# Kernel optimization log

Measured on AMD Instinct MI355X. Metric: run time of the kernel, lower is better.

Reference implementation:

```python
import jax, jax.numpy as jnp
import numpy as np

B, CDD, L, T, H, NH = 16, 10, 64, 128, 768, 12
DH = H // NH          # head dim = 64
S = CDD * L + T       # full sequence = 768 (640 candidate tokens + 128 terms)


def setup_inputs() -> dict:
    key = jax.random.key(0)
    ks = jax.random.split(key, 7)
    w = 0.02
    return {
        "hidden_states": jax.random.normal(ks[0], (B, S, H), jnp.float32),
        "Wq": jax.random.normal(ks[1], (H, H), jnp.float32) * w,
        "bq": jax.random.normal(ks[2], (H,), jnp.float32) * w,
        "Wk": jax.random.normal(ks[3], (H, H), jnp.float32) * w,
        "bk": jax.random.normal(ks[4], (H,), jnp.float32) * w,
        "Wv": jax.random.normal(ks[5], (H, H), jnp.float32) * w,
        "bv": jax.random.normal(ks[6], (H,), jnp.float32) * w,
    }


def _one_pass_mask(dtype):
    # block-diagonal over candidates + dense global columns for terms
    block = jnp.kron(jnp.eye(CDD, dtype=dtype), jnp.ones((L, L), dtype=dtype))  # [CDD*L, CDD*L]
    return jnp.concatenate([block, jnp.ones((CDD * L, T), dtype=dtype)], axis=-1)  # [CDD*L, S]


def reference(hidden_states, Wq, bq, Wk, bk, Wv, bv):
    def split_heads(x):  # [B, s, H] -> [B, NH, s, DH]
        return x.reshape(B, -1, NH, DH).transpose(0, 2, 1, 3)

    attn_field = hidden_states[:, :-T]                     # [B, CDD*L, H] queries only
    q = split_heads(attn_field @ Wq.T + bq)                # [B, NH, CDD*L, DH]
    k = split_heads(hidden_states @ Wk.T + bk)             # [B, NH, S, DH]
    v = split_heads(hidden_states @ Wv.T + bv)             # [B, NH, S, DH]

    mask = _one_pass_mask(q.dtype)                         # [CDD*L, S]
    scale = 1.0 / np.sqrt(DH).astype(np.float32)
    # NOTE: original multiplies scores by the mask (masked entries become 0, not -inf)
    scores = jnp.einsum('bhqd,bhkd->bhqk', q, k) * scale * mask
    probs = jax.nn.softmax(scores, axis=-1)                # [B, NH, CDD*L, S]

    ctx = jnp.einsum('bhqk,bhkd->bhqd', probs, v)          # [B, NH, CDD*L, DH]
    ctx = jnp.concatenate([ctx, v[:, :, -T:]], axis=2)     # append term values untouched
    return ctx.transpose(0, 2, 1, 3).reshape(B, S, H)
```

## Files before the change

### kernel.cpp

```cpp
#include <hip/hip_runtime.h>

constexpr int Bb  = 16;
constexpr int CDD = 10;
constexpr int Lc  = 64;
constexpr int T   = 128;
constexpr int H   = 768;
constexpr int NH  = 12;
constexpr int DH  = 64;
constexpr int S   = 768;
constexpr int SQ  = 640;
constexpr int MROWS = Bb * S;

typedef __attribute__((ext_vector_type(8))) short bf16x8;
typedef __attribute__((ext_vector_type(4))) short bf16x4;
typedef __attribute__((ext_vector_type(4))) float f32x4;

__device__ inline unsigned short f2bf(float f) {
  unsigned u = __float_as_uint(f);
  u += 0x7fff + ((u >> 16) & 1);
  return (unsigned short)(u >> 16);
}
__device__ inline float bf2f(unsigned short h) {
  return __uint_as_float(((unsigned)h) << 16);
}

__device__ inline void gld_lds16(const void* g, void* l) {
  __builtin_amdgcn_global_load_lds(
      (const __attribute__((address_space(1))) void*)g,
      (__attribute__((address_space(3))) void*)l, 16, 0, 0);
}

__device__ inline bf16x8 ld_b64x2(const unsigned short* p) {
  union { bf16x8 v; bf16x4 h[2]; } u;
  u.h[0] = *(const bf16x4*)p;
  u.h[1] = *(const bf16x4*)(p + 4);
  return u.v;
}

constexpr int NX4 = MROWS * H / 4;
constexpr int NW4 = H * H / 4;
__global__ void convert_all(const float* __restrict__ X,
                            const float* __restrict__ Wq,
                            const float* __restrict__ Wk,
                            const float* __restrict__ Wv,
                            unsigned short* __restrict__ Xb,
                            unsigned short* __restrict__ Wb) {
  int i = blockIdx.x * blockDim.x + threadIdx.x;
  const int stride = gridDim.x * blockDim.x;
  const int total = NX4 + 3 * NW4;
  for (; i < total; i += stride) {
    const float* src;
    unsigned short* dst;
    int off;
    if (i < NX4) {
      src = X; dst = Xb; off = i;
    } else {
      int k = i - NX4;
      int w = k / NW4;
      off = k - w * NW4;
      src = (w == 0) ? Wq : (w == 1) ? Wk : Wv;
      dst = Wb + (size_t)w * H * H;
    }
    float4 v = ((const float4*)src)[off];
    ushort4 o;
    o.x = f2bf(v.x); o.y = f2bf(v.y); o.z = f2bf(v.z); o.w = f2bf(v.w);
    ((ushort4*)dst)[off] = o;
  }
}

__launch_bounds__(512, 2)
__global__ void qkv_gemm(const unsigned short* __restrict__ Xb,
                         const unsigned short* __restrict__ Wb,
                         const float* __restrict__ bq, const float* __restrict__ bk,
                         const float* __restrict__ bv,
                         unsigned short* __restrict__ Qb, unsigned short* __restrict__ Kb,
                         unsigned short* __restrict__ Vb,
                         float* __restrict__ part,
                         float* __restrict__ out) {
  const int z  = blockIdx.y / 3;
  const int j0 = (blockIdx.y % 3) * 256;
  const int i0 = blockIdx.x * 256;
  const int xb3 = blockIdx.x % 3;
  const unsigned short* W = Wb + (size_t)z * H * H;
  const float* bias = (z == 0) ? bq : (z == 1) ? bk : bv;
  unsigned short* Y = (z == 0) ? Qb : (z == 1) ? Kb : Vb;

  const int tid = threadIdx.x;
  const int wave = tid >> 6, lane = tid & 63;
  const int wr = wave >> 2, wc = wave & 3;
  const int col = lane & 15, quad = lane >> 4;

  const bool skipHi = (z == 0) && (xb3 == 2);

  __shared__ unsigned short As0[256 * 64];
  __shared__ unsigned short As1[256 * 64];
  __shared__ unsigned short Bs0[256 * 64];
  __shared__ unsigned short Bs1[256 * 64];

  f32x4 acc[8][4];
#pragma unroll
  for (int i = 0; i < 8; i++)
#pragma unroll
    for (int j = 0; j < 4; j++) acc[i][j] = (f32x4){0.f, 0.f, 0.f, 0.f};

  bf16x8 a[4][2];
  bf16x8 b[2][2][2];

#define STAGE_HALF(src, dst, rowbase, k0, hf)                                   \
  do {                                                                          \
    _Pragma("unroll") for (int u = 0; u < 2; u++) {                             \
      const int s_ = tid + 512 * u;                                             \
      const int r_ = (s_ >> 3) + (hf) * 128;                                    \
      const int c_ = s_ & 7;                                                    \
      gld_lds16((src) + (size_t)((rowbase) + r_) * H + (k0) + ((c_ ^ (r_ & 7)) * 8), \
                &(dst)[(r_ * 8 + c_) * 8]);                                     \
    }                                                                           \
  } while (0)

#define READ_A(mh_)                                                             \
  do {                                                                          \
    _Pragma("unroll") for (int mt = 0; mt < 4; mt++) {                          \
      const int r_ = (mh_) * 128 + wr * 64 + mt * 16 + col;                     \
      _Pragma("unroll") for (int kh = 0; kh < 2; kh++)                          \
        a[mt][kh] = *(const bf16x8*)&Ar[r_ * 64 + (((kh * 4 + quad) ^ (r_ & 7)) * 8)]; \
    }                                                                           \
  } while (0)

#define READ_B(nh_)                                                             \
  do {                                                                          \
    _Pragma("unroll") for (int nf = 0; nf < 2; nf++) {                          \
      const int r_ = (nh_) * 128 + wc * 32 + nf * 16 + col;                     \
      _Pragma("unroll") for (int kh = 0; kh < 2; kh++)                          \
        b[nh_][nf][kh] = *(const bf16x8*)&Br[r_ * 64 + (((kh * 4 + quad) ^ (r_ & 7)) * 8)]; \
    }                                                                           \
  } while (0)

#define MFMA16(mh_, nh_)                                                        \
  do {                                                                          \
    __builtin_amdgcn_s_setprio(1);                                              \
    _Pragma("unroll") for (int mt = 0; mt < 4; mt++)                            \
      _Pragma("unroll") for (int nf = 0; nf < 2; nf++)                          \
        _Pragma("unroll") for (int kh = 0; kh < 2; kh++)                        \
          acc[(mh_) * 4 + mt][(nh_) * 2 + nf] =                                 \
              __builtin_amdgcn_mfma_f32_16x16x32_bf16(                          \
                  a[mt][kh], b[nh_][nf][kh], acc[(mh_) * 4 + mt][(nh_) * 2 + nf], 0, 0, 0); \
    __builtin_amdgcn_s_setprio(0);                                              \
  } while (0)

#define GATE4 asm volatile("s_waitcnt vmcnt(4)" ::: "memory")
#define GATE2 asm volatile("s_waitcnt vmcnt(2)" ::: "memory")
#define GATE0 asm volatile("s_waitcnt vmcnt(0)" ::: "memory")
#define BAR                                                                     \
  do {                                                                          \
    asm volatile("" ::: "memory");                                              \
    __builtin_amdgcn_s_barrier();                                               \
    asm volatile("" ::: "memory");                                              \
  } while (0)

  STAGE_HALF(Xb, As0, i0, 0, 0);
  STAGE_HALF(W,  Bs0, j0, 0, 0);
  STAGE_HALF(W,  Bs0, j0, 0, 1);
  STAGE_HALF(Xb, As0, i0, 0, 1);
  GATE0;
  BAR;

  for (int t = 0; t < 11; t++) {
    const unsigned short* Ar = (t & 1) ? As1 : As0;
    const unsigned short* Br = (t & 1) ? Bs1 : Bs0;
    unsigned short* Aw = (t & 1) ? As0 : As1;
    unsigned short* Bw = (t & 1) ? Bs0 : Bs1;
    const int k0n = (t + 1) * 64;

    READ_A(0); READ_B(0);
    STAGE_HALF(Xb, Aw, i0, k0n, 0);
    GATE4; BAR;
    MFMA16(0, 0);
    BAR;

    READ_B(1);
    STAGE_HALF(W, Bw, j0, k0n, 0);
    GATE4; BAR;
    MFMA16(0, 1);
    BAR;

    if (!skipHi) READ_A(1);
    STAGE_HALF(W, Bw, j0, k0n, 1);
    BAR;
    if (!skipHi) MFMA16(1, 0);
    BAR;

    STAGE_HALF(Xb, Aw, i0, k0n, 1);
    GATE4; BAR;
    if (!skipHi) MFMA16(1, 1);
    BAR;
  }

  {
    const unsigned short* Ar = As1;
    const unsigned short* Br = Bs1;
    READ_A(0); READ_B(0);
    GATE2; BAR;
    MFMA16(0, 0);
    BAR;
    READ_B(1);
    GATE0; BAR;
    MFMA16(0, 1);
    if (!skipHi) {
      READ_A(1);
      MFMA16(1, 0);
      MFMA16(1, 1);
    }
  }

  const int b_ = blockIdx.x / 3;
  float colsum[4] = {0.f, 0.f, 0.f, 0.f};
#pragma unroll
  for (int mf = 0; mf < 8; mf++) {
    if (skipHi && mf >= 4) continue;
    const int rloc = (mf >> 2) * 128 + wr * 64 + (mf & 3) * 16;
#pragma unroll
    for (int nf = 0; nf < 4; nf++) {
      const int j = j0 + (nf >> 1) * 128 + wc * 32 + (nf & 1) * 16 + col;
      const float bj = bias[j];
#pragma unroll
      for (int r = 0; r < 4; r++) {
        const int iloc = rloc + quad * 4 + r;
        const int i = i0 + iloc;
        const float v = acc[mf][nf][r] + bj;
        Y[(size_t)i * H + j] = f2bf(v);
        if (z == 2) {
          colsum[nf] += v;
          const int s = xb3 * 256 + iloc;
          if (s >= SQ) out[(size_t)i * H + j] = v;
        }
      }
    }
  }
  if (z == 2) {
#pragma unroll
    for (int nf = 0; nf < 4; nf++) {
      float s = colsum[nf];
      s += __shfl_xor(s, 16, 64);
      s += __shfl_xor(s, 32, 64);
      if (quad == 0) {
        const int j = j0 + (nf >> 1) * 128 + wc * 32 + (nf & 1) * 16 + col;
        atomicAdd(&part[b_ * H + j], s);
      }
    }
  }
#undef STAGE_HALF
#undef READ_A
#undef READ_B
#undef MFMA16
#undef GATE4
#undef GATE2
#undef GATE0
#undef BAR
}

__launch_bounds__(256, 2)
__global__ void attn_kernel(const unsigned short* __restrict__ Qb,
                            const unsigned short* __restrict__ Kb,
                            const unsigned short* __restrict__ Vb,
                            const float* __restrict__ part,
                            float* __restrict__ out) {
  const int bid = blockIdx.x;
  const int c = bid % CDD;
  const int h = (bid / CDD) % NH;
  const int b = bid / (CDD * NH);
  const int tid = threadIdx.x;
  const int wave = tid >> 6, lane = tid & 63;
  const int col = lane & 15, quad = lane >> 4;

  __shared__ __align__(16) char smem[59136];
  unsigned short* Qs = (unsigned short*)smem;
  unsigned short* Ks = (unsigned short*)(smem + 8192);
  unsigned short* Ps = (unsigned short*)smem;
  unsigned short* Vt = (unsigned short*)(smem + 32768);
  float* red   = (float*)(smem + 57856);
  float* vcorr = (float*)(smem + 58880);

  const size_t rowQ0 = (size_t)(b * S + c * 64) * H + h * DH;

  {
    int s0 = tid, s1 = tid + 256;
    int r0 = s0 >> 3, g0 = (s0 & 7) ^ (r0 & 7);
    int r1 = s1 >> 3, g1 = (s1 & 7) ^ (r1 & 7);
    gld_lds16(Qb + rowQ0 + (size_t)r0 * H + g0 * 8, &Qs[s0 * 8]);
    gld_lds16(Qb + rowQ0 + (size_t)r1 * H + g1 * 8, &Qs[s1 * 8]);
  }
#pragma unroll
  for (int j = 0; j < 6; j++) {
    int s = tid + 256 * j;
    int key = s >> 3;
    int gkey = (key < 64) ? (c * 64 + key) : (576 + key);
    int gc = (s & 7) ^ (key & 7);
    gld_lds16(Kb + (size_t)(b * S + gkey) * H + h * DH + gc * 8, &Ks[s * 8]);
  }
#pragma unroll
  for (int j = 0; j < 6; j++) {
    int s = tid + 256 * j;
    int key = s >> 3;
    int f0 = (s & 7) * 8;
    int gkey = (key < 64) ? (c * 64 + key) : (576 + key);
    union { int4 i4; unsigned short u[8]; } uv;
    uv.i4 = *(const int4*)(Vb + (size_t)(b * S + gkey) * H + h * DH + f0);
#pragma unroll
    for (int i = 0; i < 8; i++) Vt[(f0 + i) * 196 + key] = uv.u[i];
  }
  __builtin_amdgcn_s_waitcnt(0);
  __syncthreads();

  {
    int d = tid & 63, p = tid >> 6;
    float sum = 0.f;
    for (int k = p * 48; k < p * 48 + 48; k++) sum += bf2f(Vt[d * 196 + k]);
    red[tid] = sum;
  }
  __syncthreads();
  if (tid < 64) {
    float tot = part[b * H + h * DH + tid];
    vcorr[tid] = tot - (red[tid] + red[64 + tid] + red[128 + tid] + red[192 + tid]);
  }

  f32x4 sc[12];
#pragma unroll
  for (int n = 0; n < 12; n++) sc[n] = (f32x4){0.f, 0.f, 0.f, 0.f};
  {
    const int rq = wave * 16 + col;
    bf16x8 a0 = *(const bf16x8*)&Qs[rq * 64 + ((quad ^ (rq & 7)) * 8)];
    bf16x8 a1 = *(const bf16x8*)&Qs[rq * 64 + (((4 + quad) ^ (rq & 7)) * 8)];
#pragma unroll
    for (int n = 0; n < 12; n++) {
      const int rk = n * 16 + col;
      bf16x8 b0 = *(const bf16x8*)&Ks[rk * 64 + ((quad ^ (rk & 7)) * 8)];
      bf16x8 b1 = *(const bf16x8*)&Ks[rk * 64 + (((4 + quad) ^ (rk & 7)) * 8)];
      sc[n] = __builtin_amdgcn_mfma_f32_16x16x32_bf16(a0, b0, sc[n], 0, 0, 0);
      sc[n] = __builtin_amdgcn_mfma_f32_16x16x32_bf16(a1, b1, sc[n], 0, 0, 0);
    }
  }

  float em[4], zin[4];
  {
    const float scale = 0.125f;
#pragma unroll
    for (int r = 0; r < 4; r++) {
      float mx = sc[0][r];
#pragma unroll
      for (int n = 1; n < 12; n++) mx = fmaxf(mx, sc[n][r]);
#pragma unroll
      for (int msk = 1; msk <= 8; msk <<= 1) mx = fmaxf(mx, __shfl_xor(mx, msk, 64));
      const float mrow = fmaxf(mx * scale, 0.f);
      float rs = 0.f;
#pragma unroll
      for (int n = 0; n < 12; n++) {
        float p = __expf(sc[n][r] * scale - mrow);
        sc[n][r] = p;
        rs += p;
      }
#pragma unroll
      for (int msk = 1; msk <= 8; msk <<= 1) rs += __shfl_xor(rs, msk, 64);
      const float e = __expf(-mrow);
      em[r] = e;
      zin[r] = 1.f / (rs + 576.f * e);
    }
  }
  __syncthreads();

#pragma unroll
  for (int n = 0; n < 12; n++)
#pragma unroll
    for (int r = 0; r < 4; r++)
      Ps[(wave * 16 + quad * 4 + r) * 196 + n * 16 + col] = f2bf(sc[n][r]);
  __syncthreads();

  f32x4 o[4];
#pragma unroll
  for (int n2 = 0; n2 < 4; n2++) o[n2] = (f32x4){0.f, 0.f, 0.f, 0.f};
#pragma unroll
  for (int ks = 0; ks < 6; ks++) {
    bf16x8 a = ld_b64x2(&Ps[(wave * 16 + col) * 196 + ks * 32 + quad * 8]);
#pragma unroll
    for (int n2 = 0; n2 < 4; n2++) {
      bf16x8 bvv = ld_b64x2(&Vt[(n2 * 16 + col) * 196 + ks * 32 + quad * 8]);
      o[n2] = __builtin_amdgcn_mfma_f32_16x16x32_bf16(a, bvv, o[n2], 0, 0, 0);
    }
  }

#pragma unroll
  for (int n2 = 0; n2 < 4; n2++) {
    const int d = n2 * 16 + col;
    const float vc = vcorr[d];
#pragma unroll
    for (int r = 0; r < 4; r++) {
      const int m = wave * 16 + quad * 4 + r;
      const float val = (o[n2][r] + em[r] * vc) * zin[r];
      out[(size_t)(b * S + c * 64 + m) * H + h * DH + d] = val;
    }
  }
}

extern "C" void kernel_launch(void* const* d_in, const int* in_sizes, int n_in,
                              void* d_out, int out_size, void* d_ws, size_t ws_size,
                              hipStream_t stream) {
  const float* X  = (const float*)d_in[0];
  const float* Wq = (const float*)d_in[1];
  const float* bq = (const float*)d_in[2];
  const float* Wk = (const float*)d_in[3];
  const float* bk = (const float*)d_in[4];
  const float* Wv = (const float*)d_in[5];
  const float* bv = (const float*)d_in[6];
  float* out = (float*)d_out;

  char* ws = (char*)d_ws;
  unsigned short* Xb   = (unsigned short*)ws;
  unsigned short* Wb   = (unsigned short*)(ws + 18874368);
  unsigned short* Qb   = (unsigned short*)(ws + 22413312);
  unsigned short* Kb   = (unsigned short*)(ws + 41287680);
  unsigned short* Vb   = (unsigned short*)(ws + 60162048);
  float*          part = (float*)(ws + 79036416);

  hipMemsetAsync(part, 0, Bb * H * sizeof(float), stream);
  convert_all<<<2048, 256, 0, stream>>>(X, Wq, Wk, Wv, Xb, Wb);
  qkv_gemm<<<dim3(48, 9), 512, 0, stream>>>(Xb, Wb, bq, bk, bv, Qb, Kb, Vb, part, out);
  attn_kernel<<<1920, 256, 0, stream>>>(Qb, Kb, Vb, part, out);
}
```

Before: 187.5 us.

## Deepen QKV GEMM prefetch pipeline and halve barriers per phase

```diff
diff --git a/kernel.cpp b/kernel.cpp
--- a/kernel.cpp
+++ b/kernel.cpp
@@ -147,64 +147,85 @@
     __builtin_amdgcn_s_setprio(0);                                              \
   } while (0)
 
-#define GATE4 asm volatile("s_waitcnt vmcnt(4)" ::: "memory")
-#define GATE2 asm volatile("s_waitcnt vmcnt(2)" ::: "memory")
-#define GATE0 asm volatile("s_waitcnt vmcnt(0)" ::: "memory")
-#define BAR                                                                     \
-  do {                                                                          \
-    asm volatile("" ::: "memory");                                              \
+#define PHASE_SYNC(vm)                                                          \
+  do {                                                                          \
+    asm volatile("s_waitcnt vmcnt(" #vm ") lgkmcnt(0)" ::: "memory");           \
+    __builtin_amdgcn_sched_barrier(0);                                          \
     __builtin_amdgcn_s_barrier();                                               \
-    asm volatile("" ::: "memory");                                              \
+  } while (0)
+#define PHASE_SYNC_NOVM                                                         \
+  do {                                                                          \
+    asm volatile("s_waitcnt lgkmcnt(0)" ::: "memory");                          \
+    __builtin_amdgcn_sched_barrier(0);                                          \
+    __builtin_amdgcn_s_barrier();                                               \
   } while (0)
 
   STAGE_HALF(Xb, As0, i0, 0, 0);
   STAGE_HALF(W,  Bs0, j0, 0, 0);
   STAGE_HALF(W,  Bs0, j0, 0, 1);
   STAGE_HALF(Xb, As0, i0, 0, 1);
-  GATE0;
-  BAR;
-
-  for (int t = 0; t < 11; t++) {
+  STAGE_HALF(Xb, As1, i0, 64, 0);
+  STAGE_HALF(W,  Bs1, j0, 64, 0);
+  STAGE_HALF(W,  Bs1, j0, 64, 1);
+  PHASE_SYNC(10);
+
+  for (int t = 0; t < 10; t++) {
     const unsigned short* Ar = (t & 1) ? As1 : As0;
     const unsigned short* Br = (t & 1) ? Bs1 : Bs0;
-    unsigned short* Aw = (t & 1) ? As0 : As1;
-    unsigned short* Bw = (t & 1) ? Bs0 : Bs1;
-    const int k0n = (t + 1) * 64;
+    unsigned short* Acur = (t & 1) ? As1 : As0;
+    unsigned short* Bcur = (t & 1) ? Bs1 : Bs0;
+    unsigned short* Anxt = (t & 1) ? As0 : As1;
 
     READ_A(0); READ_B(0);
-    STAGE_HALF(Xb, Aw, i0, k0n, 0);
-    GATE4; BAR;
+    STAGE_HALF(Xb, Anxt, i0, (t + 1) * 64, 1);
+    PHASE_SYNC(10);
     MFMA16(0, 0);
-    BAR;
 
     READ_B(1);
-    STAGE_HALF(W, Bw, j0, k0n, 0);
-    GATE4; BAR;
+    STAGE_HALF(Xb, Acur, i0, (t + 2) * 64, 0);
+    PHASE_SYNC(10);
     MFMA16(0, 1);
-    BAR;
 
     if (!skipHi) READ_A(1);
-    STAGE_HALF(W, Bw, j0, k0n, 1);
-    BAR;
+    STAGE_HALF(W, Bcur, j0, (t + 2) * 64, 0);
+    PHASE_SYNC_NOVM;
     if (!skipHi) MFMA16(1, 0);
-    BAR;
-
-    STAGE_HALF(Xb, Aw, i0, k0n, 1);
-    GATE4; BAR;
+
+    STAGE_HALF(W, Bcur, j0, (t + 2) * 64, 1);
+    PHASE_SYNC(10);
     if (!skipHi) MFMA16(1, 1);
-    BAR;
-  }
-
+  }
+
+  {
+    const unsigned short* Ar = As0;
+    const unsigned short* Br = Bs0;
+    READ_A(0); READ_B(0);
+    STAGE_HALF(Xb, As1, i0, 11 * 64, 1);
+    PHASE_SYNC(10);
+    MFMA16(0, 0);
+
+    READ_B(1);
+    PHASE_SYNC(8);
+    MFMA16(0, 1);
+
+    if (!skipHi) READ_A(1);
+    PHASE_SYNC_NOVM;
+    if (!skipHi) MFMA16(1, 0);
+
+    PHASE_SYNC(4);
+    if (!skipHi) MFMA16(1, 1);
+  }
   {
     const unsigned short* Ar = As1;
     const unsigned short* Br = Bs1;
     READ_A(0); READ_B(0);
-    GATE2; BAR;
+    PHASE_SYNC(2);
     MFMA16(0, 0);
-    BAR;
+
     READ_B(1);
-    GATE0; BAR;
+    PHASE_SYNC(0);
     MFMA16(0, 1);
+
     if (!skipHi) {
       READ_A(1);
       MFMA16(1, 0);
@@ -252,10 +273,8 @@
 #undef READ_A
 #undef READ_B
 #undef MFMA16
-#undef GATE4
-#undef GATE2
-#undef GATE0
-#undef BAR
+#undef PHASE_SYNC
+#undef PHASE_SYNC_NOVM
 }
 
 __launch_bounds__(256, 2)
```

Result: no change. 184.4 us (-1.6%).
